# Kernel optimization log

Measured on AMD Instinct MI355X. Metric: run time of the kernel, lower is better.

## Reference

```python
import jax, jax.numpy as jnp
import numpy as np

N_NODES = 50000
N_EDGES = 1600000
IN_FEAT, H_FEAT, OUT_FEAT, N_CLASSES = 256, 128, 64, 8


def setup_inputs() -> dict:
    key = jax.random.key(0)
    ks = jax.random.split(key, 8)
    seq = jax.random.normal(ks[0], (N_NODES, IN_FEAT), dtype=jnp.float32)
    edge_index = jax.random.randint(ks[1], (2, N_EDGES), 0, N_NODES, dtype=jnp.int64)
    # GCNConv weights (stored as [in, out]) and biases; Glorot-ish scale
    W1 = jax.random.normal(ks[2], (IN_FEAT, H_FEAT), dtype=jnp.float32) / np.sqrt(IN_FEAT)
    b1 = jnp.zeros((H_FEAT,), dtype=jnp.float32)
    W2 = jax.random.normal(ks[3], (H_FEAT, OUT_FEAT), dtype=jnp.float32) / np.sqrt(H_FEAT)
    b2 = jnp.zeros((OUT_FEAT,), dtype=jnp.float32)
    Wc = jax.random.normal(ks[4], (OUT_FEAT, N_CLASSES), dtype=jnp.float32) / np.sqrt(OUT_FEAT)
    bc = jnp.zeros((N_CLASSES,), dtype=jnp.float32)
    return {"seq": seq, "edge_index": edge_index,
            "W1": W1, "b1": b1, "W2": W2, "b2": b2, "Wc": Wc, "bc": bc}


def _gcn_conv(x, W, b, src, dst, norm, n_nodes):
    # PyG GCNConv: h = x @ W, then symmetric-normalized aggregation to dst, + bias
    h = x @ W                                   # [N, out]
    msg = h[src] * norm[:, None]                # [E+N, out] gather + scale
    out = jax.ops.segment_sum(msg, dst, num_segments=n_nodes)  # scatter-add
    return out + b


def reference(seq, edge_index, W1, b1, W2, b2, Wc, bc):
    n = seq.shape[0]
    loops = jnp.arange(n, dtype=edge_index.dtype)
    src = jnp.concatenate([edge_index[0], loops])  # add self-loops
    dst = jnp.concatenate([edge_index[1], loops])
    # symmetric normalization deg^{-1/2}[src] * deg^{-1/2}[dst]
    deg = jax.ops.segment_sum(jnp.ones_like(dst, dtype=seq.dtype), dst, num_segments=n)
    dinv = jnp.where(deg > 0, jax.lax.rsqrt(deg), 0.0)
    norm = dinv[src] * dinv[dst]                  # [E+N]
    res1 = _gcn_conv(seq, W1, b1, src, dst, norm, n)
    res2 = _gcn_conv(res1, W2, b2, src, dst, norm, n)
    return res2 @ Wc + bc
```

## Files before the change

### kernel.cpp

```cpp
#include <hip/hip_runtime.h>
#include <hip/hip_bf16.h>
#include <stdint.h>

#define NN 50000
#define NE 1600000
#define BSH 7
#define NBK 391
#define CAP 4608
#define NSB 256
#define ECH 6250
#define EPAIR 3125

__global__ __launch_bounds__(1024) void k_iw(const float* __restrict__ W1, const float* __restrict__ b1,
                                             const float* __restrict__ W2, const float* __restrict__ b2,
                                             const float* __restrict__ Wc, const float* __restrict__ bc,
                                             float* __restrict__ Wcombo, float* __restrict__ c12,
                                             const int* __restrict__ dst, int* __restrict__ bh){
  const int t = threadIdx.x;
  if (blockIdx.x == 0){
    __shared__ float M1[1024];
    {
      int k = t >> 3, c = t & 7;
      float s = 0.f;
      for (int j = 0; j < 64; ++j) s += W2[k * 64 + j] * Wc[j * 8 + c];
      M1[t] = s;
    }
    __syncthreads();
    for (int idx = t; idx < 2048; idx += 1024){
      int i = idx >> 3, c = idx & 7;
      float s = 0.f;
      for (int k = 0; k < 128; ++k) s += W1[i * 128 + k] * M1[k * 8 + c];
      Wcombo[idx] = s;
    }
    if (t < 8){
      float s = 0.f;
      for (int k = 0; k < 128; ++k) s += b1[k] * M1[k * 8 + t];
      c12[t] = s;
    } else if (t < 16){
      int c = t - 8;
      float s = bc[c];
      for (int k = 0; k < 64; ++k) s += b2[k] * Wc[k * 8 + c];
      c12[t] = s;
    }
  } else {
    __shared__ int h[4 * NBK];
    const int hb = blockIdx.x - 1;
    for (int i = t; i < 4 * NBK; i += 1024) h[i] = 0;
    __syncthreads();
    const int g = (t >> 8) * NBK;
    const int2* dp = (const int2*)(dst + hb * ECH);
    for (int i = t; i < EPAIR; i += 1024){
      int2 d = dp[i];
      atomicAdd(&h[g + (d.x >> BSH)], 1);
      atomicAdd(&h[g + (d.y >> BSH)], 1);
    }
    __syncthreads();
    for (int i = t; i < NBK; i += 1024)
      bh[(size_t)hb * NBK + i] = h[i] + h[NBK + i] + h[2 * NBK + i] + h[3 * NBK + i];
  }
}

__global__ __launch_bounds__(NSB) void k_bscan(const int* __restrict__ bh, int* __restrict__ boff,
                                               int* __restrict__ btot){
  __shared__ int lds[NSB];
  const int b = blockIdx.x;
  int v = bh[(size_t)threadIdx.x * NBK + b];
  lds[threadIdx.x] = v;
  __syncthreads();
  for (int ofs = 1; ofs < NSB; ofs <<= 1){
    int t = (threadIdx.x >= ofs) ? lds[threadIdx.x - ofs] : 0;
    __syncthreads();
    lds[threadIdx.x] += t;
    __syncthreads();
  }
  boff[(size_t)threadIdx.x * NBK + b] = lds[threadIdx.x] - v;
  if (threadIdx.x == NSB - 1) btot[b] = lds[NSB - 1];
}

__global__ __launch_bounds__(1024) void k_sy(const int* __restrict__ src, const int* __restrict__ dst,
                                             const int* __restrict__ bh, const int* __restrict__ boff,
                                             uint32_t* __restrict__ ebuf,
                                             const float* __restrict__ X, const float* __restrict__ Wcombo,
                                             float* __restrict__ Yraw){
  const int t = threadIdx.x;
  if (blockIdx.x < NSB){
    __shared__ uint32_t lbuf[ECH];
    __shared__ int lcnt[NBK];
    __shared__ int lst[NBK];
    __shared__ int dbase[NBK];
    const int blk = blockIdx.x;
    int myc = 0;
    if (t < NBK){
      myc = bh[(size_t)blk * NBK + t];
      lst[t] = myc;
      lcnt[t] = 0;
      dbase[t] = t * CAP + boff[(size_t)blk * NBK + t];
    }
    __syncthreads();
    for (int ofs = 1; ofs < NBK; ofs <<= 1){
      int v = (t < NBK && t >= ofs) ? lst[t - ofs] : 0;
      __syncthreads();
      if (t < NBK) lst[t] += v;
      __syncthreads();
    }
    if (t < NBK) lst[t] -= myc;
    __syncthreads();
    const int2* dp = (const int2*)(dst + blk * ECH);
    const int2* sp = (const int2*)(src + blk * ECH);
    for (int i = t; i < EPAIR; i += 1024){
      int2 d = dp[i];
      int2 s = sp[i];
      int b0 = d.x >> BSH;
      int p0 = atomicAdd(&lcnt[b0], 1);
      lbuf[lst[b0] + p0] = ((uint32_t)s.x << 16) | (uint32_t)d.x;
      int b1i = d.y >> BSH;
      int p1 = atomicAdd(&lcnt[b1i], 1);
      lbuf[lst[b1i] + p1] = ((uint32_t)s.y << 16) | (uint32_t)d.y;
    }
    __syncthreads();
    for (int k = t; k < ECH; k += 1024){
      uint32_t v = lbuf[k];
      int b = (int)(v & 0xFFFFu) >> BSH;
      ebuf[dbase[b] + (k - lst[b])] = v;
    }
  } else {
    __shared__ float Wl[2048];
    for (int i = t; i < 2048; i += 1024) Wl[i] = Wcombo[i];
    __syncthreads();
    int gid = (blockIdx.x - NSB) * 1024 + t;
    int row = gid >> 3, c = gid & 7;
    if (row >= NN) return;
    const float* Xr = X + (size_t)row * 256;
    float acc = 0.f;
    #pragma unroll 8
    for (int k = 0; k < 256; k += 4){
      float4 x = *(const float4*)(Xr + k);
      acc += x.x * Wl[k * 8 + c] + x.y * Wl[(k + 1) * 8 + c]
           + x.z * Wl[(k + 2) * 8 + c] + x.w * Wl[(k + 3) * 8 + c];
    }
    Yraw[(size_t)row * 8 + c] = acc;
  }
}

__global__ __launch_bounds__(512) void k_csr(const uint32_t* __restrict__ ebuf, const int* __restrict__ btot,
                                             float* __restrict__ dinv, int2* __restrict__ offs2,
                                             unsigned short* __restrict__ csr){
  __shared__ uint32_t lede[CAP];
  __shared__ unsigned short lcsr[CAP];
  __shared__ int h[128];
  __shared__ int sb[128];
  const int t = threadIdx.x;
  const int b = blockIdx.x;
  const int base = b * CAP;
  const int cnt = btot[b];
  for (int i = t; i < cnt; i += 512) lede[i] = ebuf[base + i];
  if (t < 128) h[t] = 0;
  __syncthreads();
  for (int i = t; i < cnt; i += 512)
    atomicAdd(&h[lede[i] & 127], 1);
  __syncthreads();
  int deg = (t < 128) ? h[t] : 0;
  for (int ofs = 1; ofs < 128; ofs <<= 1){
    int tv = (t >= ofs && t < 128) ? h[t - ofs] : 0;
    __syncthreads();
    if (t < 128) h[t] += tv;
    __syncthreads();
  }
  int excl = (t < 128) ? (h[t] - deg) : 0;
  int node = (b << BSH) + t;
  if (t < 128 && node < NN){
    dinv[node] = rsqrtf((float)(deg + 1));
    offs2[node] = make_int2(base + excl, base + excl + deg);
  }
  __syncthreads();
  if (t < 128) sb[t] = excl;
  __syncthreads();
  for (int i = t; i < cnt; i += 512){
    uint32_t v = lede[i];
    int p = atomicAdd(&sb[v & 127], 1);
    lcsr[p] = (unsigned short)(v >> 16);
  }
  __syncthreads();
  uint32_t* dstw = (uint32_t*)(csr + base);
  const uint32_t* srcw = (const uint32_t*)lcsr;
  int nw = (cnt + 1) >> 1;
  for (int i = t; i < nw; i += 512) dstw[i] = srcw[i];
}

__global__ __launch_bounds__(256) void k_agg1(const unsigned short* __restrict__ csr, const int2* __restrict__ offs2,
                                              const float* __restrict__ dinv, const float* __restrict__ Y,
                                              float* __restrict__ U, float* __restrict__ V){
  int gid = blockIdx.x * 256 + threadIdx.x;
  int node = gid >> 3, c = gid & 7;
  if (node >= NN) return;
  int2 oe = offs2[node];
  int e = oe.x;
  const int e1 = oe.y;
  float a = 0.f, vd = 0.f;
  for (; e + 4 <= e1; e += 4){
    int s0 = csr[e], s1 = csr[e + 1], s2 = csr[e + 2], s3 = csr[e + 3];
    float d0 = dinv[s0], d1 = dinv[s1], d2 = dinv[s2], d3 = dinv[s3];
    float y0 = Y[(size_t)s0 * 8 + c], y1 = Y[(size_t)s1 * 8 + c];
    float y2 = Y[(size_t)s2 * 8 + c], y3 = Y[(size_t)s3 * 8 + c];
    a += (d0 * y0 + d1 * y1) + (d2 * y2 + d3 * y3);
    vd += (d0 + d1) + (d2 + d3);
  }
  for (; e < e1; ++e){
    int s0 = csr[e];
    float d0 = dinv[s0];
    a += d0 * Y[(size_t)s0 * 8 + c];
    vd += d0;
  }
  float di = dinv[node];
  U[(size_t)node * 8 + c] = di * di * (a + di * Y[(size_t)node * 8 + c]);
  if (c == 0) V[node] = di * (vd + di);
}

__global__ __launch_bounds__(256) void k_agg2(const unsigned short* __restrict__ csr, const int2* __restrict__ offs2,
                                              const float* __restrict__ dinv, const float* __restrict__ U,
                                              const float* __restrict__ V, const float* __restrict__ c12,
                                              float* __restrict__ O){
  int gid = blockIdx.x * 256 + threadIdx.x;
  int node = gid >> 3, c = gid & 7;
  if (node >= NN) return;
  int2 oe = offs2[node];
  int e = oe.x;
  const int e1 = oe.y;
  float a = 0.f;
  for (; e + 4 <= e1; e += 4){
    int s0 = csr[e], s1 = csr[e + 1], s2 = csr[e + 2], s3 = csr[e + 3];
    float y0 = U[(size_t)s0 * 8 + c], y1 = U[(size_t)s1 * 8 + c];
    float y2 = U[(size_t)s2 * 8 + c], y3 = U[(size_t)s3 * 8 + c];
    a += (y0 + y1) + (y2 + y3);
  }
  for (; e < e1; ++e){
    int s0 = csr[e];
    a += U[(size_t)s0 * 8 + c];
  }
  float di = dinv[node];
  O[(size_t)node * 8 + c] = di * (a + U[(size_t)node * 8 + c]) + V[node] * c12[c] + c12[8 + c];
}

extern "C" void kernel_launch(void* const* d_in, const int* in_sizes, int n_in,
                              void* d_out, int out_size, void* d_ws, size_t ws_size,
                              hipStream_t stream) {
  const float* seq = (const float*)d_in[0];
  const int*   ei  = (const int*)d_in[1];
  const int*   esrc = ei;
  const int*   edst = ei + NE;
  const float* W1 = (const float*)d_in[2];
  const float* b1 = (const float*)d_in[3];
  const float* W2 = (const float*)d_in[4];
  const float* b2 = (const float*)d_in[5];
  const float* Wc = (const float*)d_in[6];
  const float* bc = (const float*)d_in[7];
  float* out = (float*)d_out;

  char* ws = (char*)d_ws;
  size_t o = 0;
  auto alloc = [&](size_t bytes) -> void* {
    void* p = ws + o;
    o += (bytes + 255) & ~(size_t)255;
    return p;
  };
  int*      bh    = (int*)alloc((size_t)NSB * NBK * 4);
  int*      boff  = (int*)alloc((size_t)NSB * NBK * 4);
  int*      btot  = (int*)alloc((size_t)NBK * 4);
  uint32_t* ebuf  = (uint32_t*)alloc((size_t)NBK * CAP * 4);
  unsigned short* csr = (unsigned short*)alloc((size_t)NBK * CAP * 2);
  int2*     offs2 = (int2*)alloc((size_t)NN * 8);
  float*    dinv  = (float*)alloc((size_t)NN * 4);
  float*    Wcb   = (float*)alloc(2048 * 4);
  float*    c12   = (float*)alloc(16 * 4);
  float*    Yraw  = (float*)alloc((size_t)NN * 8 * 4);
  float*    U     = (float*)alloc((size_t)NN * 8 * 4);
  float*    V     = (float*)alloc((size_t)NN * 4);

  k_iw    <<<1 + NSB, 1024, 0, stream>>>(W1, b1, W2, b2, Wc, bc, Wcb, c12, edst, bh);
  k_bscan <<<NBK, NSB, 0, stream>>>(bh, boff, btot);
  k_sy    <<<NSB + 391, 1024, 0, stream>>>(esrc, edst, bh, boff, ebuf, seq, Wcb, Yraw);
  k_csr   <<<NBK, 512, 0, stream>>>(ebuf, btot, dinv, offs2, csr);
  k_agg1  <<<1563, 256, 0, stream>>>(csr, offs2, dinv, Yraw, U, V);
  k_agg2  <<<1563, 256, 0, stream>>>(csr, offs2, dinv, U, V, c12, out);
}
```

Before: 87.25 us.

## Fuse CSR build with first aggregation; move degree and X·W into separate pass

The combined scatter/GEMV kernel is split. The degree histogram (dinv) now runs in a new kernel alongside the X·Wcombo GEMV, after the edge scatter. The CSR construction kernel now also does the first-layer aggregation straight from its LDS-resident CSR, which removes the k_agg1 launch and its global re-read of the CSR. The catch is that the edge buffer is read twice, once for degrees and once in the CSR block. The fused kernel also runs only 391 blocks of 1024 threads for the gather, so it has less parallelism than 1563 blocks and may be bounded by latency.

New measurement: 88.78 us. About the same (+1.8%).

```diff
diff --git a/kernel.cpp b/kernel.cpp
--- a/kernel.cpp
+++ b/kernel.cpp
@@ -10,6 +10,7 @@
 #define NSB 256
 #define ECH 6250
 #define EPAIR 3125
+#define NYB 782
 
 __global__ __launch_bounds__(1024) void k_iw(const float* __restrict__ W1, const float* __restrict__ b1,
                                              const float* __restrict__ W2, const float* __restrict__ b2,
@@ -77,57 +78,74 @@
   if (threadIdx.x == NSB - 1) btot[b] = lds[NSB - 1];
 }
 
-__global__ __launch_bounds__(1024) void k_sy(const int* __restrict__ src, const int* __restrict__ dst,
-                                             const int* __restrict__ bh, const int* __restrict__ boff,
-                                             uint32_t* __restrict__ ebuf,
-                                             const float* __restrict__ X, const float* __restrict__ Wcombo,
-                                             float* __restrict__ Yraw){
+__global__ __launch_bounds__(1024) void k_scat(const int* __restrict__ src, const int* __restrict__ dst,
+                                               const int* __restrict__ bh, const int* __restrict__ boff,
+                                               uint32_t* __restrict__ ebuf){
+  __shared__ uint32_t lbuf[ECH];
+  __shared__ int lcnt[NBK];
+  __shared__ int lst[NBK];
+  __shared__ int dbase[NBK];
   const int t = threadIdx.x;
-  if (blockIdx.x < NSB){
-    __shared__ uint32_t lbuf[ECH];
-    __shared__ int lcnt[NBK];
-    __shared__ int lst[NBK];
-    __shared__ int dbase[NBK];
-    const int blk = blockIdx.x;
-    int myc = 0;
-    if (t < NBK){
-      myc = bh[(size_t)blk * NBK + t];
-      lst[t] = myc;
-      lcnt[t] = 0;
-      dbase[t] = t * CAP + boff[(size_t)blk * NBK + t];
-    }
-    __syncthreads();
-    for (int ofs = 1; ofs < NBK; ofs <<= 1){
-      int v = (t < NBK && t >= ofs) ? lst[t - ofs] : 0;
-      __syncthreads();
-      if (t < NBK) lst[t] += v;
-      __syncthreads();
-    }
-    if (t < NBK) lst[t] -= myc;
-    __syncthreads();
-    const int2* dp = (const int2*)(dst + blk * ECH);
-    const int2* sp = (const int2*)(src + blk * ECH);
-    for (int i = t; i < EPAIR; i += 1024){
-      int2 d = dp[i];
-      int2 s = sp[i];
-      int b0 = d.x >> BSH;
-      int p0 = atomicAdd(&lcnt[b0], 1);
-      lbuf[lst[b0] + p0] = ((uint32_t)s.x << 16) | (uint32_t)d.x;
-      int b1i = d.y >> BSH;
-      int p1 = atomicAdd(&lcnt[b1i], 1);
-      lbuf[lst[b1i] + p1] = ((uint32_t)s.y << 16) | (uint32_t)d.y;
-    }
-    __syncthreads();
-    for (int k = t; k < ECH; k += 1024){
-      uint32_t v = lbuf[k];
-      int b = (int)(v & 0xFFFFu) >> BSH;
-      ebuf[dbase[b] + (k - lst[b])] = v;
-    }
+  const int blk = blockIdx.x;
+  int myc = 0;
+  if (t < NBK){
+    myc = bh[(size_t)blk * NBK + t];
+    lst[t] = myc;
+    lcnt[t] = 0;
+    dbase[t] = t * CAP + boff[(size_t)blk * NBK + t];
+  }
+  __syncthreads();
+  for (int ofs = 1; ofs < NBK; ofs <<= 1){
+    int v = (t < NBK && t >= ofs) ? lst[t - ofs] : 0;
+    __syncthreads();
+    if (t < NBK) lst[t] += v;
+    __syncthreads();
+  }
+  if (t < NBK) lst[t] -= myc;
+  __syncthreads();
+  const int2* dp = (const int2*)(dst + blk * ECH);
+  const int2* sp = (const int2*)(src + blk * ECH);
+  for (int i = t; i < EPAIR; i += 1024){
+    int2 d = dp[i];
+    int2 s = sp[i];
+    int b0 = d.x >> BSH;
+    int p0 = atomicAdd(&lcnt[b0], 1);
+    lbuf[lst[b0] + p0] = ((uint32_t)s.x << 16) | (uint32_t)d.x;
+    int b1i = d.y >> BSH;
+    int p1 = atomicAdd(&lcnt[b1i], 1);
+    lbuf[lst[b1i] + p1] = ((uint32_t)s.y << 16) | (uint32_t)d.y;
+  }
+  __syncthreads();
+  for (int k = t; k < ECH; k += 1024){
+    uint32_t v = lbuf[k];
+    int b = (int)(v & 0xFFFFu) >> BSH;
+    ebuf[dbase[b] + (k - lst[b])] = v;
+  }
+}
+
+__global__ __launch_bounds__(512) void k_dy(const uint32_t* __restrict__ ebuf, const int* __restrict__ btot,
+                                            float* __restrict__ dinv,
+                                            const float* __restrict__ X, const float* __restrict__ Wcombo,
+                                            float* __restrict__ Yraw){
+  const int t = threadIdx.x;
+  if (blockIdx.x < NBK){
+    __shared__ int h[128];
+    const int b = blockIdx.x;
+    const int base = b * CAP;
+    const int cnt = btot[b];
+    if (t < 128) h[t] = 0;
+    __syncthreads();
+    for (int e = base + t; e < base + cnt; e += 512)
+      atomicAdd(&h[ebuf[e] & 127], 1);
+    __syncthreads();
+    int node = (b << BSH) + t;
+    if (t < 128 && node < NN)
+      dinv[node] = rsqrtf((float)(h[t] + 1));
   } else {
     __shared__ float Wl[2048];
-    for (int i = t; i < 2048; i += 1024) Wl[i] = Wcombo[i];
-    __syncthreads();
-    int gid = (blockIdx.x - NSB) * 1024 + t;
+    for (int i = t; i < 2048; i += 512) Wl[i] = Wcombo[i];
+    __syncthreads();
+    int gid = (blockIdx.x - NBK) * 512 + t;
     int row = gid >> 3, c = gid & 7;
     if (row >= NN) return;
     const float* Xr = X + (size_t)row * 256;
@@ -142,21 +160,23 @@
   }
 }
 
-__global__ __launch_bounds__(512) void k_csr(const uint32_t* __restrict__ ebuf, const int* __restrict__ btot,
-                                             float* __restrict__ dinv, int2* __restrict__ offs2,
-                                             unsigned short* __restrict__ csr){
+__global__ __launch_bounds__(1024) void k_csrA1(const uint32_t* __restrict__ ebuf, const int* __restrict__ btot,
+                                                const float* __restrict__ dinv, const float* __restrict__ Y,
+                                                int2* __restrict__ offs2, unsigned short* __restrict__ csr,
+                                                float* __restrict__ U, float* __restrict__ V){
   __shared__ uint32_t lede[CAP];
   __shared__ unsigned short lcsr[CAP];
   __shared__ int h[128];
   __shared__ int sb[128];
+  __shared__ int hst[128];
   const int t = threadIdx.x;
   const int b = blockIdx.x;
   const int base = b * CAP;
   const int cnt = btot[b];
-  for (int i = t; i < cnt; i += 512) lede[i] = ebuf[base + i];
+  for (int i = t; i < cnt; i += 1024) lede[i] = ebuf[base + i];
   if (t < 128) h[t] = 0;
   __syncthreads();
-  for (int i = t; i < cnt; i += 512)
+  for (int i = t; i < cnt; i += 1024)
     atomicAdd(&h[lede[i] & 127], 1);
   __syncthreads();
   int deg = (t < 128) ? h[t] : 0;
@@ -168,52 +188,49 @@
   }
   int excl = (t < 128) ? (h[t] - deg) : 0;
   int node = (b << BSH) + t;
-  if (t < 128 && node < NN){
-    dinv[node] = rsqrtf((float)(deg + 1));
+  if (t < 128 && node < NN)
     offs2[node] = make_int2(base + excl, base + excl + deg);
-  }
-  __syncthreads();
-  if (t < 128) sb[t] = excl;
-  __syncthreads();
-  for (int i = t; i < cnt; i += 512){
+  __syncthreads();
+  if (t < 128){ sb[t] = excl; hst[t] = excl; }
+  __syncthreads();
+  for (int i = t; i < cnt; i += 1024){
     uint32_t v = lede[i];
     int p = atomicAdd(&sb[v & 127], 1);
     lcsr[p] = (unsigned short)(v >> 16);
   }
   __syncthreads();
-  uint32_t* dstw = (uint32_t*)(csr + base);
-  const uint32_t* srcw = (const uint32_t*)lcsr;
-  int nw = (cnt + 1) >> 1;
-  for (int i = t; i < nw; i += 512) dstw[i] = srcw[i];
-}
-
-__global__ __launch_bounds__(256) void k_agg1(const unsigned short* __restrict__ csr, const int2* __restrict__ offs2,
-                                              const float* __restrict__ dinv, const float* __restrict__ Y,
-                                              float* __restrict__ U, float* __restrict__ V){
-  int gid = blockIdx.x * 256 + threadIdx.x;
-  int node = gid >> 3, c = gid & 7;
-  if (node >= NN) return;
-  int2 oe = offs2[node];
-  int e = oe.x;
-  const int e1 = oe.y;
-  float a = 0.f, vd = 0.f;
-  for (; e + 4 <= e1; e += 4){
-    int s0 = csr[e], s1 = csr[e + 1], s2 = csr[e + 2], s3 = csr[e + 3];
-    float d0 = dinv[s0], d1 = dinv[s1], d2 = dinv[s2], d3 = dinv[s3];
-    float y0 = Y[(size_t)s0 * 8 + c], y1 = Y[(size_t)s1 * 8 + c];
-    float y2 = Y[(size_t)s2 * 8 + c], y3 = Y[(size_t)s3 * 8 + c];
-    a += (d0 * y0 + d1 * y1) + (d2 * y2 + d3 * y3);
-    vd += (d0 + d1) + (d2 + d3);
-  }
-  for (; e < e1; ++e){
-    int s0 = csr[e];
-    float d0 = dinv[s0];
-    a += d0 * Y[(size_t)s0 * 8 + c];
-    vd += d0;
-  }
-  float di = dinv[node];
-  U[(size_t)node * 8 + c] = di * di * (a + di * Y[(size_t)node * 8 + c]);
-  if (c == 0) V[node] = di * (vd + di);
+  {
+    uint32_t* dstw = (uint32_t*)(csr + base);
+    const uint32_t* srcw = (const uint32_t*)lcsr;
+    int nw = (cnt + 1) >> 1;
+    for (int i = t; i < nw; i += 1024) dstw[i] = srcw[i];
+  }
+  {
+    int ln = t >> 3, c = t & 7;
+    int nd = (b << BSH) + ln;
+    if (nd < NN){
+      int e = hst[ln];
+      const int e1 = e + (sb[ln] - hst[ln]);
+      float a = 0.f, vd = 0.f;
+      for (; e + 4 <= e1; e += 4){
+        int s0 = lcsr[e], s1 = lcsr[e + 1], s2 = lcsr[e + 2], s3 = lcsr[e + 3];
+        float d0 = dinv[s0], d1 = dinv[s1], d2 = dinv[s2], d3 = dinv[s3];
+        float y0 = Y[(size_t)s0 * 8 + c], y1 = Y[(size_t)s1 * 8 + c];
+        float y2 = Y[(size_t)s2 * 8 + c], y3 = Y[(size_t)s3 * 8 + c];
+        a += (d0 * y0 + d1 * y1) + (d2 * y2 + d3 * y3);
+        vd += (d0 + d1) + (d2 + d3);
+      }
+      for (; e < e1; ++e){
+        int s0 = lcsr[e];
+        float d0 = dinv[s0];
+        a += d0 * Y[(size_t)s0 * 8 + c];
+        vd += d0;
+      }
+      float di = dinv[nd];
+      U[(size_t)nd * 8 + c] = di * di * (a + di * Y[(size_t)nd * 8 + c]);
+      if (c == 0) V[nd] = di * (vd + di);
+    }
+  }
 }
 
 __global__ __launch_bounds__(256) void k_agg2(const unsigned short* __restrict__ csr, const int2* __restrict__ offs2,
@@ -278,8 +295,8 @@
 
   k_iw    <<<1 + NSB, 1024, 0, stream>>>(W1, b1, W2, b2, Wc, bc, Wcb, c12, edst, bh);
   k_bscan <<<NBK, NSB, 0, stream>>>(bh, boff, btot);
-  k_sy    <<<NSB + 391, 1024, 0, stream>>>(esrc, edst, bh, boff, ebuf, seq, Wcb, Yraw);
-  k_csr   <<<NBK, 512, 0, stream>>>(ebuf, btot, dinv, offs2, csr);
-  k_agg1  <<<1563, 256, 0, stream>>>(csr, offs2, dinv, Yraw, U, V);
+  k_scat  <<<NSB, 1024, 0, stream>>>(esrc, edst, bh, boff, ebuf);
+  k_dy    <<<NBK + NYB, 512, 0, stream>>>(ebuf, btot, dinv, seq, Wcb, Yraw);
+  k_csrA1 <<<NBK, 1024, 0, stream>>>(ebuf, btot, dinv, Yraw, offs2, csr, U, V);
   k_agg2  <<<1563, 256, 0, stream>>>(csr, offs2, dinv, U, V, c12, out);
 }
```
